# Performance work log

Hardware: AMD Instinct MI355X
Metric: run time of the kernel (lower is better)

Reference implementation:

```python
import jax, jax.numpy as jnp
from jax import lax
import numpy as np

B_, T_ = 16, 8
H_, W_ = 14, 14
h_, w_ = 3, 3
N_ = h_ * w_
CB, C_, D_ = 1024, 512, 128


def setup_inputs():
    key = jax.random.key(0)
    ks = jax.random.split(key, 16)
    rn = lambda i, shp, s=0.02: jax.random.normal(ks[i], shp, dtype=jnp.float32) * s
    z = lambda *s: jnp.zeros(s, jnp.float32)
    o = lambda *s: jnp.ones(s, jnp.float32)
    return {
        'x': jax.random.normal(ks[0], (B_ * T_, CB, H_, W_), dtype=jnp.float32),
        'W_proj': rn(1, (C_, CB)), 'b_proj': z(C_),
        'W_attn': rn(2, (N_, C_)),
        'W_gf': rn(3, (D_, C_)), 'b_gf': z(D_),
        'g1': o(N_, D_), 'beta1': z(N_, D_), 'g2': o(N_, D_), 'beta2': z(N_, D_),
        'W_ih': rn(4, (4 * D_, D_)), 'W_hh': rn(5, (4 * D_, D_)), 'b_ih': z(4 * D_), 'b_hh': z(4 * D_),
        'W_pred': rn(6, (4, D_)), 'b_pred': z(4), 'alpha': jnp.full((4,), 0.5, jnp.float32),
        'W_kp1': rn(7, (C_, H_ * W_)), 'b_kp1': z(C_),
        'Wq': rn(8, (C_, C_)), 'Wk': rn(9, (C_, C_)), 'Wv': rn(10, (C_, C_)), 'Wu': rn(11, (C_, C_)), 'b_u': z(C_),
        'W_gih': rn(12, (3 * C_, C_)), 'W_ghh': rn(13, (3 * C_, C_)), 'b_gih': z(3 * C_), 'b_ghh': z(3 * C_),
        'W_back': rn(14, (CB, C_)), 'b_back': z(CB),
    }


def _ln(x, g, b, eps=1e-5):
    m = x.mean(-1, keepdims=True)
    v = x.var(-1, keepdims=True)
    return (x - m) / jnp.sqrt(v + eps) * g + b


def _forward(x, W_proj, b_proj, W_attn, W_gf, b_gf, g1, beta1, g2, beta2, W_ih, W_hh, b_ih, b_hh, W_pred, b_pred, alpha, W_kp1, b_kp1, Wq, Wk, Wv, Wu, b_u, W_gih, W_ghh, b_gih, b_ghh, W_back, b_back):
    BT = x.shape[0]
    # 1x1 conv projection backbone_dim -> node_dim (project_at_input)  [BT, C, H, W]
    feat = jnp.einsum('oc,bchw->bohw', W_proj, x) + b_proj[None, :, None, None]
    # offset generator: per-node attention pooling over space (GloRe-style)
    logits = jnp.einsum('nc,bchw->bnhw', W_attn, feat).reshape(BT, N_, H_ * W_)
    attw = jax.nn.softmax(logits, axis=-1).reshape(BT, N_, H_, W_)
    gf = jnp.einsum('bnhw,bchw->bnc', attw, feat)  # [BT, N, C]
    gf = _ln(gf @ W_gf.T + b_gf, g1, beta1)  # [BT, N, D]
    # temporal LSTM over T, batched over (B, node)
    xs = gf.reshape(B_, T_, N_, D_).transpose(1, 0, 2, 3).reshape(T_, B_ * N_, D_)
    def lstm_step(carry, xt):
        hp, cp = carry
        gates = xt @ W_ih.T + b_ih + hp @ W_hh.T + b_hh
        i, f, gg, oo = jnp.split(gates, 4, axis=-1)
        c = jax.nn.sigmoid(f) * cp + jax.nn.sigmoid(i) * jnp.tanh(gg)
        hn = jax.nn.sigmoid(oo) * jnp.tanh(c)
        return (hn, c), hn
    h0 = jnp.zeros((B_ * N_, D_), xs.dtype)
    _, ys = lax.scan(lstm_step, (h0, h0), xs)
    ys = ys.reshape(T_, B_, N_, D_).transpose(1, 0, 2, 3).reshape(BT, N_, D_)
    off = (_ln(ys, g2, beta2) @ W_pred.T + b_pred) * alpha  # [BT, N, 4]
    # grid anchors (init_regions='grid'): centers at (k+0.5)*H/h
    ph0 = (jnp.arange(h_, dtype=x.dtype) + 0.5) * (H_ / h_)
    pw0 = (jnp.arange(w_, dtype=x.dtype) + 0.5) * (W_ / w_)
    ch = jnp.repeat(ph0, w_)[None] + off[..., 0]
    cw = jnp.tile(pw0, h_)[None] + off[..., 1]
    sh = (H_ / h_) * jnp.exp(off[..., 2])
    sw = (W_ / w_) * jnp.exp(off[..., 3])
    rel_h = (jnp.arange(h_, dtype=x.dtype) + 0.5) / h_ - 0.5
    rel_w = (jnp.arange(w_, dtype=x.dtype) + 0.5) / w_ - 0.5
    pos_h = ch[..., None] + sh[..., None] * rel_h  # [BT, N, h]
    pos_w = cw[..., None] + sw[..., None] * rel_w  # [BT, N, w]
    grid_h = jnp.arange(H_, dtype=x.dtype)
    grid_w = jnp.arange(W_, dtype=x.dtype)
    kh = jax.nn.relu(1.0 - jnp.abs(pos_h[..., None] - grid_h))  # [BT, N, h, H] linear-interp kernels
    kw = jax.nn.relu(1.0 - jnp.abs(pos_w[..., None] - grid_w))  # [BT, N, w, W]
    # differentiable crop: sample h x w region per node, pool to node vector
    t1 = jnp.einsum('bniH,bcHL->bnicL', kh, feat)
    samp = jnp.einsum('bnicL,bnjL->bnicj', t1, kw).mean(axis=(2, 4))  # [BT, N, C]
    # kernel-location embedding (kernel_projection1), combine_by_sum
    kern2d = jnp.einsum('bniH,bnjL->bnHL', kh, kw).reshape(BT, N_, H_ * W_)
    nodes = samp + kern2d @ W_kp1.T + b_kp1
    # RSTG: spatial message passing on fully-connected node graph
    nd = nodes.reshape(B_, T_, N_, C_)
    q = nd @ Wq.T
    k = nd @ Wk.T
    v = nd @ Wv.T
    att = jax.nn.softmax(jnp.einsum('btic,btjc->btij', q, k) / jnp.sqrt(jnp.asarray(C_, x.dtype)), axis=-1)
    agg = jnp.einsum('btij,btjc->btic', att, v)
    nd = nd + jax.nn.relu(agg @ Wu.T + b_u)
    # RSTG: temporal GRU per node
    def gru_step(hp, xt):
        gi = xt @ W_gih.T + b_gih
        gh = hp @ W_ghh.T + b_ghh
        ir, iz, ig = jnp.split(gi, 3, axis=-1)
        hr, hz, hg = jnp.split(gh, 3, axis=-1)
        r = jax.nn.sigmoid(ir + hr)
        zz = jax.nn.sigmoid(iz + hz)
        n = jnp.tanh(ig + r * hg)
        hn = (1.0 - zz) * n + zz * hp
        return hn, hn
    g0 = jnp.zeros((B_, N_, C_), x.dtype)
    _, hs = lax.scan(gru_step, g0, nd.transpose(1, 0, 2, 3))
    out_nodes = hs.transpose(1, 0, 2, 3).reshape(BT, N_, C_)
    # remap node states back to the spatial map with the same kernels
    khs = kh.sum(2)  # [BT, N, H]
    kws = kw.sum(2)  # [BT, N, W]
    num = jnp.einsum('bnc,bnH,bnL->bcHL', out_nodes, khs, kws)
    den = jnp.einsum('bnH,bnL->bHL', khs, kws) + 1e-6
    out_map = num / den[:, None]
    # project back node_dim -> backbone_dim (project_back_i3d_linear), residual add
    return x + jnp.einsum('oc,bchw->bohw', W_back, out_map) + b_back[None, :, None, None]


def reference(x, W_proj, b_proj, W_attn, W_gf, b_gf, g1, beta1, g2, beta2, W_ih, W_hh, b_ih, b_hh, W_pred, b_pred, alpha, W_kp1, b_kp1, Wq, Wk, Wv, Wu, b_u, W_gih, W_ghh, b_gih, b_ghh, W_back, b_back):
    return _forward(x, W_proj, b_proj, W_attn, W_gf, b_gf, g1, beta1, g2, beta2, W_ih, W_hh, b_ih, b_hh, W_pred, b_pred, alpha, W_kp1, b_kp1, Wq, Wk, Wv, Wu, b_u, W_gih, W_ghh, b_gih, b_ghh, W_back, b_back)
```

## Files before the change

kernel.cpp:

```cpp
#include <hip/hip_runtime.h>

typedef unsigned short u16;
typedef __attribute__((ext_vector_type(8))) u16 b16x8;
typedef __attribute__((ext_vector_type(4))) float f32x4;

static constexpr int HWn = 196;
static constexpr int NN  = 9;
static constexpr int Cn  = 512;
static constexpr int CBn = 1024;
static constexpr int Dn  = 128;
static constexpr int BTn = 128;

__device__ __forceinline__ float sigm(float x) { return 1.f / (1.f + expf(-x)); }

__device__ __forceinline__ u16 f2bf(float f) {
  unsigned int u = __builtin_bit_cast(unsigned int, f);
  u = (u + 0x7fff + ((u >> 16) & 1)) >> 16;
  return (u16)u;
}

__device__ __forceinline__ float waveSum(float v) {
#pragma unroll
  for (int o = 32; o > 0; o >>= 1) v += __shfl_down(v, o, 64);
  return v;
}
__device__ __forceinline__ float waveMax(float v) {
#pragma unroll
  for (int o = 32; o > 0; o >>= 1) v = fmaxf(v, __shfl_down(v, o, 64));
  return v;
}
__device__ __forceinline__ float blockSum(float v, float* red) {
  const int lane = threadIdx.x & 63, wid = threadIdx.x >> 6;
  const int nw = blockDim.x >> 6;
  v = waveSum(v);
  __syncthreads();
  if (lane == 0) red[wid] = v;
  __syncthreads();
  float r = 0.f;
  for (int i = 0; i < nw; ++i) r += red[i];
  return r;
}
__device__ __forceinline__ float blockMax(float v, float* red) {
  const int lane = threadIdx.x & 63, wid = threadIdx.x >> 6;
  const int nw = blockDim.x >> 6;
  v = waveMax(v);
  __syncthreads();
  if (lane == 0) red[wid] = v;
  __syncthreads();
  float r = -3.4e38f;
  for (int i = 0; i < nw; ++i) r = fmaxf(r, red[i]);
  return r;
}

__global__ __launch_bounds__(256) void k_cast(const float* __restrict__ in,
                                              u16* __restrict__ out, int n) {
  const int i = (blockIdx.x * 256 + threadIdx.x) * 4;
  if (i < n) {
    const float4 v = *(const float4*)&in[i];
    out[i + 0] = f2bf(v.x); out[i + 1] = f2bf(v.y);
    out[i + 2] = f2bf(v.z); out[i + 3] = f2bf(v.w);
  }
}

__global__ __launch_bounds__(256) void k_xt(const float* __restrict__ x,
                                            u16* __restrict__ xT) {
  __shared__ u16 T[64][201];
  const int bt = blockIdx.x, c0 = blockIdx.y * 64, tid = threadIdx.x;
  const float* xb = x + ((size_t)bt * CBn + c0) * HWn;
  for (int idx = tid; idx < 64 * HWn; idx += 256)
    T[idx / HWn][idx % HWn] = f2bf(xb[idx]);
  __syncthreads();
  unsigned int* xTu = (unsigned int*)(xT + ((size_t)bt * HWn) * CBn + c0);
  for (int idx = tid; idx < HWn * 32; idx += 256) {
    const int hw = idx >> 5, j = idx & 31;
    const unsigned int lo = T[2 * j][hw], hi = T[2 * j + 1][hw];
    xTu[(size_t)hw * (CBn / 2) + j] = lo | (hi << 16);
  }
}

template <int MODE>
__global__ __launch_bounds__(256) void k_mm128(const u16* __restrict__ A,
                                               const u16* __restrict__ B,
                                               const float* __restrict__ bias,
                                               const float* __restrict__ xres,
                                               float* __restrict__ C,
                                               const int M, const int N, const int K) {
  __shared__ __align__(16) u16 As[128 * 64];
  __shared__ __align__(16) u16 Bs[128 * 64];
  const int tid = threadIdx.x;
  const int lane = tid & 63;
  const int w = tid >> 6, wr = w >> 1, wc = w & 1;
  const int m0 = blockIdx.x * 128, n0 = blockIdx.y * 128;

  int srow[4], slds[4], sc16[4];
#pragma unroll
  for (int i = 0; i < 4; ++i) {
    const int chunk = i * 256 + tid;
    const int row = chunk >> 3, c16 = chunk & 7;
    srow[i] = row; sc16[i] = c16;
    slds[i] = row * 64 + ((c16 ^ (row & 7)) << 3);
  }
  uint4 ar[4], br[4];
#pragma unroll
  for (int i = 0; i < 4; ++i) {
    ar[i] = *(const uint4*)(A + (size_t)(m0 + srow[i]) * K + sc16[i] * 8);
    br[i] = *(const uint4*)(B + (size_t)(n0 + srow[i]) * K + sc16[i] * 8);
  }

  int fa[4][2], fb[4][2];
#pragma unroll
  for (int q = 0; q < 4; ++q)
#pragma unroll
    for (int ks = 0; ks < 2; ++ks) {
      const int rowa = wr * 64 + q * 16 + (lane & 15);
      fa[q][ks] = rowa * 64 + (((ks * 4 + (lane >> 4)) ^ (rowa & 7)) << 3);
      const int rowb = wc * 64 + q * 16 + (lane & 15);
      fb[q][ks] = rowb * 64 + (((ks * 4 + (lane >> 4)) ^ (rowb & 7)) << 3);
    }

  f32x4 acc[4][4];
#pragma unroll
  for (int a = 0; a < 4; ++a)
#pragma unroll
    for (int b = 0; b < 4; ++b) acc[a][b] = f32x4{0.f, 0.f, 0.f, 0.f};

  for (int k0 = 0; k0 < K; k0 += 64) {
    __syncthreads();
#pragma unroll
    for (int i = 0; i < 4; ++i) {
      *(uint4*)&As[slds[i]] = ar[i];
      *(uint4*)&Bs[slds[i]] = br[i];
    }
    __syncthreads();
    const int kn = k0 + 64;
    if (kn < K) {
#pragma unroll
      for (int i = 0; i < 4; ++i) {
        ar[i] = *(const uint4*)(A + (size_t)(m0 + srow[i]) * K + kn + sc16[i] * 8);
        br[i] = *(const uint4*)(B + (size_t)(n0 + srow[i]) * K + kn + sc16[i] * 8);
      }
    }
    b16x8 af[4][2], bg[4][2];
#pragma unroll
    for (int q = 0; q < 4; ++q)
#pragma unroll
      for (int ks = 0; ks < 2; ++ks) {
        af[q][ks] = *(const b16x8*)&As[fa[q][ks]];
        bg[q][ks] = *(const b16x8*)&Bs[fb[q][ks]];
      }
#pragma unroll
    for (int ks = 0; ks < 2; ++ks)
#pragma unroll
      for (int mi = 0; mi < 4; ++mi)
#pragma unroll
        for (int nj = 0; nj < 4; ++nj)
          asm volatile("v_mfma_f32_16x16x32_bf16 %0, %1, %2, %0"
                       : "+v"(acc[mi][nj])
                       : "v"(af[mi][ks]), "v"(bg[nj][ks]));
  }

#pragma unroll
  for (int nj = 0; nj < 4; ++nj) {
    const int n = n0 + wc * 64 + nj * 16 + (lane & 15);
    const float bv = bias[n];
#pragma unroll
    for (int mi = 0; mi < 4; ++mi) {
#pragma unroll
      for (int r = 0; r < 4; ++r) {
        const int m = m0 + wr * 64 + mi * 16 + (lane >> 4) * 4 + r;
        if (MODE == 0) {
          C[(size_t)m * N + n] = acc[mi][nj][r] + bv;
        } else {
          const int b = m / HWn, hw = m - b * HWn;
          const size_t adr = ((size_t)b * CBn + n) * HWn + hw;
          C[adr] = xres[adr] + acc[mi][nj][r] + bv;
        }
      }
    }
  }
}

template <int BIAS, int RELU, int RESID>
__global__ __launch_bounds__(256) void k_gemm(const float* __restrict__ A,
                                              const float* __restrict__ W,
                                              const float* __restrict__ bias,
                                              const float* __restrict__ resid,
                                              float* __restrict__ C,
                                              int M, int N, int K) {
  __shared__ __align__(16) float As[16][68];
  __shared__ __align__(16) float Ws[16][68];
  const int m0 = blockIdx.x * 64, n0 = blockIdx.y * 64;
  const int tid = threadIdx.x, tn = tid & 15, tm = tid >> 4;
  const int lr = tid >> 2, lc4 = (tid & 3) << 2;
  float acc[4][4] = {};
  for (int k0 = 0; k0 < K; k0 += 16) {
    float4 a = make_float4(0.f, 0.f, 0.f, 0.f);
    if (m0 + lr < M) a = *(const float4*)&A[(size_t)(m0 + lr) * K + k0 + lc4];
    As[lc4 + 0][lr] = a.x; As[lc4 + 1][lr] = a.y; As[lc4 + 2][lr] = a.z; As[lc4 + 3][lr] = a.w;
    const float4 w = *(const float4*)&W[(size_t)(n0 + lr) * K + k0 + lc4];
    Ws[lc4 + 0][lr] = w.x; Ws[lc4 + 1][lr] = w.y; Ws[lc4 + 2][lr] = w.z; Ws[lc4 + 3][lr] = w.w;
    __syncthreads();
#pragma unroll
    for (int k = 0; k < 16; ++k) {
      const float4 a4 = *(const float4*)&As[k][tm << 2];
      const float4 b4 = *(const float4*)&Ws[k][tn << 2];
      const float av[4] = {a4.x, a4.y, a4.z, a4.w};
      const float bv[4] = {b4.x, b4.y, b4.z, b4.w};
#pragma unroll
      for (int i = 0; i < 4; ++i)
#pragma unroll
        for (int j = 0; j < 4; ++j) acc[i][j] += av[i] * bv[j];
    }
    __syncthreads();
  }
#pragma unroll
  for (int i = 0; i < 4; ++i) {
    const int m = m0 + tm * 4 + i;
    if (m >= M) continue;
    const int n = n0 + tn * 4;
    float4 v = make_float4(acc[i][0], acc[i][1], acc[i][2], acc[i][3]);
    if (BIAS) { v.x += bias[n]; v.y += bias[n + 1]; v.z += bias[n + 2]; v.w += bias[n + 3]; }
    if (RELU) {
      v.x = fmaxf(v.x, 0.f); v.y = fmaxf(v.y, 0.f);
      v.z = fmaxf(v.z, 0.f); v.w = fmaxf(v.w, 0.f);
    }
    if (RESID) {
      const float4 rr = *(const float4*)&resid[(size_t)m * N + n];
      v.x += rr.x; v.y += rr.y; v.z += rr.z; v.w += rr.w;
    }
    *(float4*)&C[(size_t)m * N + n] = v;
  }
}

__global__ __launch_bounds__(256) void k_attnpool(const float* __restrict__ feat,
                                                  const float* __restrict__ Wattn,
                                                  float* __restrict__ attw) {
  __shared__ float S[HWn][65];
  __shared__ float Wa[NN][64];
  __shared__ float L[NN][HWn];
  __shared__ float red[4];
  const int bt = blockIdx.x, tid = threadIdx.x;
  float lacc[NN];
#pragma unroll
  for (int n = 0; n < NN; ++n) lacc[n] = 0.f;
  const float* fb = feat + (size_t)bt * HWn * Cn;
  const int srow = tid >> 4, sc4 = (tid & 15) << 2;
  for (int c0 = 0; c0 < Cn; c0 += 64) {
    for (int rr = srow; rr < HWn; rr += 16) {
      const float4 f = *(const float4*)&fb[(size_t)rr * Cn + c0 + sc4];
      S[rr][sc4] = f.x; S[rr][sc4 + 1] = f.y; S[rr][sc4 + 2] = f.z; S[rr][sc4 + 3] = f.w;
    }
    for (int idx = tid; idx < NN * 64; idx += 256)
      Wa[idx >> 6][idx & 63] = Wattn[(size_t)(idx >> 6) * Cn + c0 + (idx & 63)];
    __syncthreads();
    if (tid < HWn) {
      for (int c = 0; c < 64; ++c) {
        const float s = S[tid][c];
#pragma unroll
        for (int n = 0; n < NN; ++n) lacc[n] += Wa[n][c] * s;
      }
    }
    __syncthreads();
  }
  if (tid < HWn)
#pragma unroll
    for (int n = 0; n < NN; ++n) L[n][tid] = lacc[n];
  __syncthreads();
  for (int n = 0; n < NN; ++n) {
    const float v = (tid < HWn) ? L[n][tid] : -3.4e38f;
    const float mx = blockMax(v, red);
    const float e = (tid < HWn) ? expf(v - mx) : 0.f;
    const float s = blockSum(e, red);
    if (tid < HWn) attw[((size_t)bt * NN + n) * HWn + tid] = e / s;
  }
}

__global__ __launch_bounds__(256) void k_gf(const float* __restrict__ feat,
                                            const float* __restrict__ attw,
                                            float* __restrict__ gf) {
  __shared__ float aw[NN][HWn];
  const int bt = blockIdx.x, tid = threadIdx.x;
  for (int idx = tid; idx < NN * HWn; idx += 256)
    aw[idx / HWn][idx % HWn] = attw[(size_t)bt * NN * HWn + idx];
  __syncthreads();
  float a0[NN] = {}, a1[NN] = {};
  const float* fb = feat + (size_t)bt * HWn * Cn;
  for (int hw = 0; hw < HWn; ++hw) {
    const float f0 = fb[(size_t)hw * Cn + tid];
    const float f1 = fb[(size_t)hw * Cn + tid + 256];
#pragma unroll
    for (int n = 0; n < NN; ++n) {
      const float w = aw[n][hw];
      a0[n] += w * f0; a1[n] += w * f1;
    }
  }
#pragma unroll
  for (int n = 0; n < NN; ++n) {
    gf[((size_t)bt * NN + n) * Cn + tid] = a0[n];
    gf[((size_t)bt * NN + n) * Cn + tid + 256] = a1[n];
  }
}

__global__ __launch_bounds__(128) void k_gfln(const float* __restrict__ gf,
                                              const float* __restrict__ Wgf,
                                              const float* __restrict__ bgf,
                                              const float* __restrict__ g1,
                                              const float* __restrict__ beta1,
                                              float* __restrict__ gf2) {
  __shared__ __align__(16) float src[Cn];
  __shared__ float red[4];
  const int row = blockIdx.x;
  const int n = row % NN;
  const int tid = threadIdx.x;
  for (int i = tid; i < Cn; i += 128) src[i] = gf[(size_t)row * Cn + i];
  __syncthreads();
  float acc = bgf[tid];
  const float* wr = Wgf + (size_t)tid * Cn;
  for (int c = 0; c < Cn; c += 4) {
    const float4 w = *(const float4*)&wr[c];
    acc += w.x * src[c] + w.y * src[c + 1] + w.z * src[c + 2] + w.w * src[c + 3];
  }
  const float mean = blockSum(acc, red) * (1.f / 128.f);
  const float d = acc - mean;
  const float var = blockSum(d * d, red) * (1.f / 128.f);
  gf2[(size_t)row * Dn + tid] =
      d * rsqrtf(var + 1e-5f) * g1[n * Dn + tid] + beta1[n * Dn + tid];
}

__global__ __launch_bounds__(256) void k_lstm(const float* __restrict__ xW,
                                              const float* __restrict__ Whh,
                                              const float* __restrict__ bhh,
                                              float* __restrict__ ys) {
  __shared__ __align__(16) float h[Dn];
  __shared__ float cc[Dn];
  __shared__ float gates[4 * Dn];
  const int blk = blockIdx.x, b = blk / NN, n = blk % NN;
  const int tid = threadIdx.x;
  if (tid < Dn) { h[tid] = 0.f; cc[tid] = 0.f; }
  __syncthreads();
  for (int t = 0; t < 8; ++t) {
    const int bt = b * 8 + t;
    const size_t xrow = ((size_t)bt * NN + n) * (4 * Dn);
#pragma unroll
    for (int gq = 0; gq < 2; ++gq) {
      const int g = tid + gq * 256;
      float acc = xW[xrow + g] + bhh[g];
      const float* wr = Whh + (size_t)g * Dn;
#pragma unroll 8
      for (int d = 0; d < Dn; d += 4) {
        const float4 w = *(const float4*)&wr[d];
        acc += w.x * h[d] + w.y * h[d + 1] + w.z * h[d + 2] + w.w * h[d + 3];
      }
      gates[g] = acc;
    }
    __syncthreads();
    if (tid < Dn) {
      const float ig = sigm(gates[tid]);
      const float fg = sigm(gates[Dn + tid]);
      const float gg = tanhf(gates[2 * Dn + tid]);
      const float og = sigm(gates[3 * Dn + tid]);
      const float cn = fg * cc[tid] + ig * gg;
      const float hn = og * tanhf(cn);
      cc[tid] = cn; h[tid] = hn;
      ys[((size_t)bt * NN + n) * Dn + tid] = hn;
    }
    __syncthreads();
  }
}

__global__ __launch_bounds__(128) void k_off(const float* __restrict__ ys,
                                             const float* __restrict__ g2,
                                             const float* __restrict__ beta2,
                                             const float* __restrict__ Wpred,
                                             const float* __restrict__ bpred,
                                             const float* __restrict__ alpha,
                                             float* __restrict__ khs,
                                             float* __restrict__ kws) {
  __shared__ float red[4];
  __shared__ float cpar[4];
  const int row = blockIdx.x;
  const int n = row % NN;
  const int tid = threadIdx.x;
  const float y = ys[(size_t)row * Dn + tid];
  const float mean = blockSum(y, red) * (1.f / 128.f);
  const float d = y - mean;
  const float var = blockSum(d * d, red) * (1.f / 128.f);
  const float v = d * rsqrtf(var + 1e-5f) * g2[n * Dn + tid] + beta2[n * Dn + tid];
  const float o0 = blockSum(v * Wpred[0 * Dn + tid], red);
  const float o1 = blockSum(v * Wpred[1 * Dn + tid], red);
  const float o2 = blockSum(v * Wpred[2 * Dn + tid], red);
  const float o3 = blockSum(v * Wpred[3 * Dn + tid], red);
  if (tid == 0) {
    const float f0 = (o0 + bpred[0]) * alpha[0];
    const float f1 = (o1 + bpred[1]) * alpha[1];
    const float f2 = (o2 + bpred[2]) * alpha[2];
    const float f3 = (o3 + bpred[3]) * alpha[3];
    const float ph0 = ((n / 3) + 0.5f) * (14.f / 3.f);
    const float pw0 = ((n % 3) + 0.5f) * (14.f / 3.f);
    cpar[0] = ph0 + f0;
    cpar[1] = pw0 + f1;
    cpar[2] = (14.f / 3.f) * expf(f2);
    cpar[3] = (14.f / 3.f) * expf(f3);
  }
  __syncthreads();
  if (tid < 14) {
    float s = 0.f;
#pragma unroll
    for (int i = 0; i < 3; ++i) {
      const float rel = (i + 0.5f) / 3.f - 0.5f;
      const float p = cpar[0] + cpar[2] * rel;
      s += fmaxf(1.f - fabsf(p - (float)tid), 0.f);
    }
    khs[(size_t)row * 14 + tid] = s;
  } else if (tid < 28) {
    const int H = tid - 14;
    float s = 0.f;
#pragma unroll
    for (int i = 0; i < 3; ++i) {
      const float rel = (i + 0.5f) / 3.f - 0.5f;
      const float p = cpar[1] + cpar[3] * rel;
      s += fmaxf(1.f - fabsf(p - (float)H), 0.f);
    }
    kws[(size_t)row * 14 + H] = s;
  }
}

__global__ __launch_bounds__(256) void k_wkp1t(const float* __restrict__ Wkp1,
                                               float* __restrict__ wkT) {
  const int hw = blockIdx.x, c = threadIdx.x;
  wkT[(size_t)hw * Cn + c] = Wkp1[(size_t)c * HWn + hw];
  wkT[(size_t)hw * Cn + c + 256] = Wkp1[(size_t)(c + 256) * HWn + hw];
}

__global__ __launch_bounds__(256) void k_nodes(const float* __restrict__ feat,
                                               const float* __restrict__ wkT,
                                               const float* __restrict__ khs,
                                               const float* __restrict__ kws,
                                               const float* __restrict__ bkp1,
                                               float* __restrict__ nodes) {
  __shared__ float kh[NN][14], kw[NN][14];
  const int bt = blockIdx.x, tid = threadIdx.x;
  if (tid < NN * 14) {
    kh[tid / 14][tid % 14] = khs[(size_t)bt * NN * 14 + tid];
    kw[tid / 14][tid % 14] = kws[(size_t)bt * NN * 14 + tid];
  }
  __syncthreads();
  float a0[NN] = {}, a1[NN] = {};
  const float* fb = feat + (size_t)bt * HWn * Cn;
  for (int hw = 0; hw < HWn; ++hw) {
    const int Hh = hw / 14, Ll = hw % 14;
    const float f0 = fb[(size_t)hw * Cn + tid] * (1.f / 9.f) + wkT[(size_t)hw * Cn + tid];
    const float f1 = fb[(size_t)hw * Cn + tid + 256] * (1.f / 9.f) + wkT[(size_t)hw * Cn + tid + 256];
#pragma unroll
    for (int n = 0; n < NN; ++n) {
      const float w = kh[n][Hh] * kw[n][Ll];
      a0[n] += w * f0; a1[n] += w * f1;
    }
  }
#pragma unroll
  for (int n = 0; n < NN; ++n) {
    nodes[((size_t)bt * NN + n) * Cn + tid] = a0[n] + bkp1[tid];
    nodes[((size_t)bt * NN + n) * Cn + tid + 256] = a1[n] + bkp1[tid + 256];
  }
}

__global__ __launch_bounds__(256) void k_att(const float* __restrict__ q,
                                             const float* __restrict__ k,
                                             const float* __restrict__ v,
                                             float* __restrict__ agg) {
  __shared__ __align__(16) float qs[NN][Cn];
  __shared__ __align__(16) float ks[NN][Cn];
  __shared__ __align__(16) float vs[NN][Cn];
  __shared__ float s[NN][NN];
  const int bt = blockIdx.x, tid = threadIdx.x;
  const size_t base = (size_t)bt * NN * Cn;
  for (int idx = tid; idx < NN * Cn; idx += 256) {
    qs[idx / Cn][idx % Cn] = q[base + idx];
    ks[idx / Cn][idx % Cn] = k[base + idx];
    vs[idx / Cn][idx % Cn] = v[base + idx];
  }
  __syncthreads();
  if (tid < NN * NN) {
    const int i = tid / NN, j = tid % NN;
    float acc = 0.f;
    for (int c = 0; c < Cn; c += 4) {
      const float4 qa = *(const float4*)&qs[i][c];
      const float4 kb = *(const float4*)&ks[j][c];
      acc += qa.x * kb.x + qa.y * kb.y + qa.z * kb.z + qa.w * kb.w;
    }
    s[i][j] = acc * 0.044194173824159216f;
  }
  __syncthreads();
  if (tid < NN) {
    float mx = -3.4e38f;
#pragma unroll
    for (int j = 0; j < NN; ++j) mx = fmaxf(mx, s[tid][j]);
    float sum = 0.f;
#pragma unroll
    for (int j = 0; j < NN; ++j) { const float e = expf(s[tid][j] - mx); s[tid][j] = e; sum += e; }
    const float inv = 1.f / sum;
#pragma unroll
    for (int j = 0; j < NN; ++j) s[tid][j] *= inv;
  }
  __syncthreads();
  for (int c = tid; c < Cn; c += 256) {
#pragma unroll
    for (int i = 0; i < NN; ++i) {
      float acc = 0.f;
#pragma unroll
      for (int j = 0; j < NN; ++j) acc += s[i][j] * vs[j][c];
      agg[((size_t)bt * NN + i) * Cn + c] = acc;
    }
  }
}

template <int T0>
__global__ __launch_bounds__(256) void k_gruupd(const float* __restrict__ gi,
                                                const float* __restrict__ gh,
                                                const float* __restrict__ bghh,
                                                float* __restrict__ hgru,
                                                float* __restrict__ out_nodes,
                                                int t) {
  const int idx = blockIdx.x * 256 + threadIdx.x;
  const int row = idx >> 9, d = idx & 511;
  const int b = row / NN, n = row % NN;
  const size_t girow = ((size_t)(b * 8 + t) * NN + n) * (3 * Cn);
  const float ir = gi[girow + d], iz = gi[girow + Cn + d], ig = gi[girow + 2 * Cn + d];
  float hr, hz, hg, hp;
  if (T0) {
    hr = bghh[d]; hz = bghh[Cn + d]; hg = bghh[2 * Cn + d]; hp = 0.f;
  } else {
    const size_t gr = (size_t)row * (3 * Cn);
    hr = gh[gr + d]; hz = gh[gr + Cn + d]; hg = gh[gr + 2 * Cn + d];
    hp = hgru[(size_t)row * Cn + d];
  }
  const float rg = sigm(ir + hr);
  const float zg = sigm(iz + hz);
  const float ng = tanhf(ig + rg * hg);
  const float h = (1.f - zg) * ng + zg * hp;
  hgru[(size_t)row * Cn + d] = h;
  out_nodes[((size_t)(b * 8 + t) * NN + n) * Cn + d] = h;
}

__global__ __launch_bounds__(256) void k_remap(const float* __restrict__ out_nodes,
                                               const float* __restrict__ khs,
                                               const float* __restrict__ kws,
                                               u16* __restrict__ om) {
  __shared__ __align__(16) float on[NN][Cn];
  __shared__ float kh[NN][14], kw[NN][14];
  const int bt = blockIdx.x, tid = threadIdx.x;
  for (int idx = tid; idx < NN * Cn; idx += 256)
    on[idx / Cn][idx % Cn] = out_nodes[(size_t)bt * NN * Cn + idx];
  if (tid < NN * 14) {
    kh[tid / 14][tid % 14] = khs[(size_t)bt * NN * 14 + tid];
    kw[tid / 14][tid % 14] = kws[(size_t)bt * NN * 14 + tid];
  }
  __syncthreads();
  for (int hw = 0; hw < HWn; ++hw) {
    const int Hh = hw / 14, Ll = hw % 14;
    float w[NN];
    float den = 1e-6f;
#pragma unroll
    for (int n = 0; n < NN; ++n) { w[n] = kh[n][Hh] * kw[n][Ll]; den += w[n]; }
    const float inv = 1.f / den;
    float s0 = 0.f, s1 = 0.f;
#pragma unroll
    for (int n = 0; n < NN; ++n) {
      s0 += on[n][tid] * w[n];
      s1 += on[n][tid + 256] * w[n];
    }
    om[((size_t)bt * HWn + hw) * Cn + tid] = f2bf(s0 * inv);
    om[((size_t)bt * HWn + hw) * Cn + tid + 256] = f2bf(s1 * inv);
  }
}

extern "C" void kernel_launch(void* const* d_in, const int* in_sizes, int n_in,
                              void* d_out, int out_size, void* d_ws, size_t ws_size,
                              hipStream_t stream) {
  const float* x      = (const float*)d_in[0];
  const float* W_proj = (const float*)d_in[1];
  const float* b_proj = (const float*)d_in[2];
  const float* W_attn = (const float*)d_in[3];
  const float* W_gf   = (const float*)d_in[4];
  const float* b_gf   = (const float*)d_in[5];
  const float* g1     = (const float*)d_in[6];
  const float* beta1  = (const float*)d_in[7];
  const float* g2     = (const float*)d_in[8];
  const float* beta2  = (const float*)d_in[9];
  const float* W_ih   = (const float*)d_in[10];
  const float* W_hh   = (const float*)d_in[11];
  const float* b_ih   = (const float*)d_in[12];
  const float* b_hh   = (const float*)d_in[13];
  const float* W_pred = (const float*)d_in[14];
  const float* b_pred = (const float*)d_in[15];
  const float* alpha  = (const float*)d_in[16];
  const float* W_kp1  = (const float*)d_in[17];
  const float* b_kp1  = (const float*)d_in[18];
  const float* Wq     = (const float*)d_in[19];
  const float* Wk     = (const float*)d_in[20];
  const float* Wv     = (const float*)d_in[21];
  const float* Wu     = (const float*)d_in[22];
  const float* b_u    = (const float*)d_in[23];
  const float* W_gih  = (const float*)d_in[24];
  const float* W_ghh  = (const float*)d_in[25];
  const float* b_gih  = (const float*)d_in[26];
  const float* b_ghh  = (const float*)d_in[27];
  const float* W_back = (const float*)d_in[28];
  const float* b_back = (const float*)d_in[29];
  float* out = (float*)d_out;

  float* ws = (float*)d_ws;
  float* feat = ws;
  u16* om16 = (u16*)feat;
  float* pool = ws + 12845056;
  u16* xT = (u16*)pool;
  size_t off = 0;
  float* attw      = pool + off; off += (size_t)BTn * NN * HWn;
  float* gf        = pool + off; off += (size_t)BTn * NN * Cn;
  float* gf2       = pool + off; off += (size_t)BTn * NN * Dn;
  float* xW        = pool + off; off += (size_t)BTn * NN * 512;
  float* ys        = pool + off; off += (size_t)BTn * NN * Dn;
  float* khs       = pool + off; off += (size_t)BTn * NN * 14;
  float* kws       = pool + off; off += (size_t)BTn * NN * 14;
  float* nodes     = pool + off; off += (size_t)BTn * NN * Cn;
  float* qb        = pool + off; off += (size_t)BTn * NN * Cn;
  float* kb        = pool + off; off += (size_t)BTn * NN * Cn;
  float* vb        = pool + off; off += (size_t)BTn * NN * Cn;
  float* aggb      = pool + off; off += (size_t)BTn * NN * Cn;
  float* nd2       = pool + off; off += (size_t)BTn * NN * Cn;
  float* gi        = pool + off; off += (size_t)BTn * NN * 3 * Cn;
  float* hgru      = pool + off; off += (size_t)144 * Cn;
  float* gh        = pool + off; off += (size_t)144 * 3 * Cn;
  float* wkT       = pool + off; off += (size_t)HWn * Cn;
  float* out_nodes = pool + off; off += (size_t)BTn * NN * Cn;
  u16* Wpb = (u16*)(ws + 25690112);
  u16* Wbb = (u16*)(ws + 25952256);

  k_cast<<<512, 256, 0, stream>>>(W_proj, Wpb, 524288);
  k_cast<<<512, 256, 0, stream>>>(W_back, Wbb, 524288);
  k_xt<<<dim3(128, 16), 256, 0, stream>>>(x, xT);
  k_mm128<0><<<dim3(196, 4), 256, 0, stream>>>(xT, Wpb, b_proj, nullptr, feat, 25088, 512, 1024);
  k_attnpool<<<BTn, 256, 0, stream>>>(feat, W_attn, attw);
  k_gf<<<BTn, 256, 0, stream>>>(feat, attw, gf);
  k_gfln<<<BTn * NN, 128, 0, stream>>>(gf, W_gf, b_gf, g1, beta1, gf2);
  k_gemm<1, 0, 0><<<dim3(18, 8), 256, 0, stream>>>(gf2, W_ih, b_ih, nullptr, xW, 1152, 512, 128);
  k_lstm<<<144, 256, 0, stream>>>(xW, W_hh, b_hh, ys);
  k_off<<<BTn * NN, 128, 0, stream>>>(ys, g2, beta2, W_pred, b_pred, alpha, khs, kws);
  k_wkp1t<<<HWn, 256, 0, stream>>>(W_kp1, wkT);
  k_nodes<<<BTn, 256, 0, stream>>>(feat, wkT, khs, kws, b_kp1, nodes);
  k_gemm<0, 0, 0><<<dim3(18, 8), 256, 0, stream>>>(nodes, Wq, nullptr, nullptr, qb, 1152, 512, 512);
  k_gemm<0, 0, 0><<<dim3(18, 8), 256, 0, stream>>>(nodes, Wk, nullptr, nullptr, kb, 1152, 512, 512);
  k_gemm<0, 0, 0><<<dim3(18, 8), 256, 0, stream>>>(nodes, Wv, nullptr, nullptr, vb, 1152, 512, 512);
  k_att<<<BTn, 256, 0, stream>>>(qb, kb, vb, aggb);
  k_gemm<1, 1, 1><<<dim3(18, 8), 256, 0, stream>>>(aggb, Wu, b_u, nodes, nd2, 1152, 512, 512);
  k_gemm<1, 0, 0><<<dim3(18, 24), 256, 0, stream>>>(nd2, W_gih, b_gih, nullptr, gi, 1152, 1536, 512);
  for (int t = 0; t < 8; ++t) {
    if (t > 0)
      k_gemm<1, 0, 0><<<dim3(3, 24), 256, 0, stream>>>(hgru, W_ghh, b_ghh, nullptr, gh, 144, 1536, 512);
    if (t == 0)
      k_gruupd<1><<<288, 256, 0, stream>>>(gi, gh, b_ghh, hgru, out_nodes, t);
    else
      k_gruupd<0><<<288, 256, 0, stream>>>(gi, gh, b_ghh, hgru, out_nodes, t);
  }
  k_remap<<<BTn, 256, 0, stream>>>(out_nodes, khs, kws, om16);
  k_mm128<1><<<dim3(196, 8), 256, 0, stream>>>(om16, Wbb, b_back, x, out, 25088, 1024, 512);
}
```

Measured before the change: 1.377 ms.

## Route mid-size fp32 GEMMs through bf16 MFMA kernel with fused epilogues

Replaces the scalar fp32 tiled GEMM used for the LSTM input projection, Q/K/V/U projections, GRU input gates and per-step GRU hidden GEMM with the bf16 MFMA 128x128 kernel. Adds one combined cast kernel for the mid-stage weights, makes producer kernels also emit bf16 copies of their outputs, and adds an M-bound clamp plus a bias/ReLU/residual epilogue that writes bf16. The MODE 1 back-projection epilogue swaps the MFMA operand order so each lane writes consecutive spatial positions. The gain is tensor-core throughput and less traffic; the cost is extra cast work, bf16 precision loss in the recurrent GRU, and underfilled grids (36 to 108 blocks).

Result: slower. 1.431 ms (+3.9%).

```diff
diff --git a/kernel.cpp b/kernel.cpp
--- a/kernel.cpp
+++ b/kernel.cpp
@@ -62,6 +62,30 @@
   }
 }
 
+__global__ __launch_bounds__(256) void k_castall(const float* __restrict__ wq,
+                                                 const float* __restrict__ wk,
+                                                 const float* __restrict__ wv,
+                                                 const float* __restrict__ wu,
+                                                 const float* __restrict__ wgih,
+                                                 const float* __restrict__ wghh,
+                                                 const float* __restrict__ wih,
+                                                 u16* __restrict__ dst) {
+  const int i = (blockIdx.x * 256 + threadIdx.x) * 4;
+  if (i >= 2686976) return;
+  const float* src;
+  int o = i;
+  if (i < 262144) { src = wq; }
+  else if (i < 524288)  { src = wk;   o = i - 262144; }
+  else if (i < 786432)  { src = wv;   o = i - 524288; }
+  else if (i < 1048576) { src = wu;   o = i - 786432; }
+  else if (i < 1835008) { src = wgih; o = i - 1048576; }
+  else if (i < 2621440) { src = wghh; o = i - 1835008; }
+  else                  { src = wih;  o = i - 2621440; }
+  const float4 v = *(const float4*)&src[o];
+  dst[i + 0] = f2bf(v.x); dst[i + 1] = f2bf(v.y);
+  dst[i + 2] = f2bf(v.z); dst[i + 3] = f2bf(v.w);
+}
+
 __global__ __launch_bounds__(256) void k_xt(const float* __restrict__ x,
                                             u16* __restrict__ xT) {
   __shared__ u16 T[64][201];
@@ -82,7 +106,7 @@
 __global__ __launch_bounds__(256) void k_mm128(const u16* __restrict__ A,
                                                const u16* __restrict__ B,
                                                const float* __restrict__ bias,
-                                               const float* __restrict__ xres,
+                                               const float* __restrict__ resid,
                                                float* __restrict__ C,
                                                const int M, const int N, const int K) {
   __shared__ __align__(16) u16 As[128 * 64];
@@ -92,19 +116,21 @@
   const int w = tid >> 6, wr = w >> 1, wc = w & 1;
   const int m0 = blockIdx.x * 128, n0 = blockIdx.y * 128;
 
-  int srow[4], slds[4], sc16[4];
+  int srowA[4], srowB[4], slds[4], sc16[4];
 #pragma unroll
   for (int i = 0; i < 4; ++i) {
     const int chunk = i * 256 + tid;
     const int row = chunk >> 3, c16 = chunk & 7;
-    srow[i] = row; sc16[i] = c16;
+    srowA[i] = min(m0 + row, M - 1);
+    srowB[i] = n0 + row;
+    sc16[i] = c16;
     slds[i] = row * 64 + ((c16 ^ (row & 7)) << 3);
   }
   uint4 ar[4], br[4];
 #pragma unroll
   for (int i = 0; i < 4; ++i) {
-    ar[i] = *(const uint4*)(A + (size_t)(m0 + srow[i]) * K + sc16[i] * 8);
-    br[i] = *(const uint4*)(B + (size_t)(n0 + srow[i]) * K + sc16[i] * 8);
+    ar[i] = *(const uint4*)(A + (size_t)srowA[i] * K + sc16[i] * 8);
+    br[i] = *(const uint4*)(B + (size_t)srowB[i] * K + sc16[i] * 8);
   }
 
   int fa[4][2], fb[4][2];
@@ -136,8 +162,8 @@
     if (kn < K) {
 #pragma unroll
       for (int i = 0; i < 4; ++i) {
-        ar[i] = *(const uint4*)(A + (size_t)(m0 + srow[i]) * K + kn + sc16[i] * 8);
-        br[i] = *(const uint4*)(B + (size_t)(n0 + srow[i]) * K + kn + sc16[i] * 8);
+        ar[i] = *(const uint4*)(A + (size_t)srowA[i] * K + kn + sc16[i] * 8);
+        br[i] = *(const uint4*)(B + (size_t)srowB[i] * K + kn + sc16[i] * 8);
       }
     }
     b16x8 af[4][2], bg[4][2];
@@ -153,82 +179,54 @@
 #pragma unroll
       for (int mi = 0; mi < 4; ++mi)
 #pragma unroll
-        for (int nj = 0; nj < 4; ++nj)
-          asm volatile("v_mfma_f32_16x16x32_bf16 %0, %1, %2, %0"
-                       : "+v"(acc[mi][nj])
-                       : "v"(af[mi][ks]), "v"(bg[nj][ks]));
-  }
-
-#pragma unroll
-  for (int nj = 0; nj < 4; ++nj) {
-    const int n = n0 + wc * 64 + nj * 16 + (lane & 15);
-    const float bv = bias[n];
-#pragma unroll
-    for (int mi = 0; mi < 4; ++mi) {
+        for (int nj = 0; nj < 4; ++nj) {
+          if (MODE == 1)
+            asm volatile("v_mfma_f32_16x16x32_bf16 %0, %1, %2, %0"
+                         : "+v"(acc[mi][nj])
+                         : "v"(bg[nj][ks]), "v"(af[mi][ks]));
+          else
+            asm volatile("v_mfma_f32_16x16x32_bf16 %0, %1, %2, %0"
+                         : "+v"(acc[mi][nj])
+                         : "v"(af[mi][ks]), "v"(bg[nj][ks]));
+        }
+  }
+
+  if (MODE == 1) {
+#pragma unroll
+    for (int nj = 0; nj < 4; ++nj) {
 #pragma unroll
       for (int r = 0; r < 4; ++r) {
-        const int m = m0 + wr * 64 + mi * 16 + (lane >> 4) * 4 + r;
-        if (MODE == 0) {
-          C[(size_t)m * N + n] = acc[mi][nj][r] + bv;
-        } else {
+        const int n = n0 + wc * 64 + nj * 16 + (lane >> 4) * 4 + r;
+        const float bv = bias[n];
+#pragma unroll
+        for (int mi = 0; mi < 4; ++mi) {
+          const int m = m0 + wr * 64 + mi * 16 + (lane & 15);
           const int b = m / HWn, hw = m - b * HWn;
           const size_t adr = ((size_t)b * CBn + n) * HWn + hw;
-          C[adr] = xres[adr] + acc[mi][nj][r] + bv;
+          C[adr] = resid[adr] + acc[mi][nj][r] + bv;
         }
       }
     }
-  }
-}
-
-template <int BIAS, int RELU, int RESID>
-__global__ __launch_bounds__(256) void k_gemm(const float* __restrict__ A,
-                                              const float* __restrict__ W,
-                                              const float* __restrict__ bias,
-                                              const float* __restrict__ resid,
-                                              float* __restrict__ C,
-                                              int M, int N, int K) {
-  __shared__ __align__(16) float As[16][68];
-  __shared__ __align__(16) float Ws[16][68];
-  const int m0 = blockIdx.x * 64, n0 = blockIdx.y * 64;
-  const int tid = threadIdx.x, tn = tid & 15, tm = tid >> 4;
-  const int lr = tid >> 2, lc4 = (tid & 3) << 2;
-  float acc[4][4] = {};
-  for (int k0 = 0; k0 < K; k0 += 16) {
-    float4 a = make_float4(0.f, 0.f, 0.f, 0.f);
-    if (m0 + lr < M) a = *(const float4*)&A[(size_t)(m0 + lr) * K + k0 + lc4];
-    As[lc4 + 0][lr] = a.x; As[lc4 + 1][lr] = a.y; As[lc4 + 2][lr] = a.z; As[lc4 + 3][lr] = a.w;
-    const float4 w = *(const float4*)&W[(size_t)(n0 + lr) * K + k0 + lc4];
-    Ws[lc4 + 0][lr] = w.x; Ws[lc4 + 1][lr] = w.y; Ws[lc4 + 2][lr] = w.z; Ws[lc4 + 3][lr] = w.w;
-    __syncthreads();
-#pragma unroll
-    for (int k = 0; k < 16; ++k) {
-      const float4 a4 = *(const float4*)&As[k][tm << 2];
-      const float4 b4 = *(const float4*)&Ws[k][tn << 2];
-      const float av[4] = {a4.x, a4.y, a4.z, a4.w};
-      const float bv[4] = {b4.x, b4.y, b4.z, b4.w};
-#pragma unroll
-      for (int i = 0; i < 4; ++i)
-#pragma unroll
-        for (int j = 0; j < 4; ++j) acc[i][j] += av[i] * bv[j];
-    }
-    __syncthreads();
-  }
-#pragma unroll
-  for (int i = 0; i < 4; ++i) {
-    const int m = m0 + tm * 4 + i;
-    if (m >= M) continue;
-    const int n = n0 + tn * 4;
-    float4 v = make_float4(acc[i][0], acc[i][1], acc[i][2], acc[i][3]);
-    if (BIAS) { v.x += bias[n]; v.y += bias[n + 1]; v.z += bias[n + 2]; v.w += bias[n + 3]; }
-    if (RELU) {
-      v.x = fmaxf(v.x, 0.f); v.y = fmaxf(v.y, 0.f);
-      v.z = fmaxf(v.z, 0.f); v.w = fmaxf(v.w, 0.f);
-    }
-    if (RESID) {
-      const float4 rr = *(const float4*)&resid[(size_t)m * N + n];
-      v.x += rr.x; v.y += rr.y; v.z += rr.z; v.w += rr.w;
-    }
-    *(float4*)&C[(size_t)m * N + n] = v;
+  } else {
+#pragma unroll
+    for (int nj = 0; nj < 4; ++nj) {
+      const int n = n0 + wc * 64 + nj * 16 + (lane & 15);
+      const float bv = (MODE == 3) ? bias[n] : (bias ? bias[n] : 0.f);
+#pragma unroll
+      for (int mi = 0; mi < 4; ++mi) {
+#pragma unroll
+        for (int r = 0; r < 4; ++r) {
+          const int m = m0 + wr * 64 + mi * 16 + (lane >> 4) * 4 + r;
+          if (m >= M) continue;
+          if (MODE == 0) {
+            C[(size_t)m * N + n] = acc[mi][nj][r] + bv;
+          } else {
+            const float val = resid[(size_t)m * N + n] + fmaxf(acc[mi][nj][r] + bv, 0.f);
+            ((u16*)C)[(size_t)m * N + n] = f2bf(val);
+          }
+        }
+      }
+    }
   }
 }
 
@@ -306,7 +304,7 @@
                                               const float* __restrict__ bgf,
                                               const float* __restrict__ g1,
                                               const float* __restrict__ beta1,
-                                              float* __restrict__ gf2) {
+                                              u16* __restrict__ gf2b) {
   __shared__ __align__(16) float src[Cn];
   __shared__ float red[4];
   const int row = blockIdx.x;
@@ -323,8 +321,8 @@
   const float mean = blockSum(acc, red) * (1.f / 128.f);
   const float d = acc - mean;
   const float var = blockSum(d * d, red) * (1.f / 128.f);
-  gf2[(size_t)row * Dn + tid] =
-      d * rsqrtf(var + 1e-5f) * g1[n * Dn + tid] + beta1[n * Dn + tid];
+  gf2b[(size_t)row * Dn + tid] =
+      f2bf(d * rsqrtf(var + 1e-5f) * g1[n * Dn + tid] + beta1[n * Dn + tid]);
 }
 
 __global__ __launch_bounds__(256) void k_lstm(const float* __restrict__ xW,
@@ -437,7 +435,8 @@
                                                const float* __restrict__ khs,
                                                const float* __restrict__ kws,
                                                const float* __restrict__ bkp1,
-                                               float* __restrict__ nodes) {
+                                               float* __restrict__ nodes,
+                                               u16* __restrict__ nodesb) {
   __shared__ float kh[NN][14], kw[NN][14];
   const int bt = blockIdx.x, tid = threadIdx.x;
   if (tid < NN * 14) {
@@ -459,15 +458,19 @@
   }
 #pragma unroll
   for (int n = 0; n < NN; ++n) {
-    nodes[((size_t)bt * NN + n) * Cn + tid] = a0[n] + bkp1[tid];
-    nodes[((size_t)bt * NN + n) * Cn + tid + 256] = a1[n] + bkp1[tid + 256];
+    const float v0 = a0[n] + bkp1[tid];
+    const float v1 = a1[n] + bkp1[tid + 256];
+    nodes[((size_t)bt * NN + n) * Cn + tid] = v0;
+    nodes[((size_t)bt * NN + n) * Cn + tid + 256] = v1;
+    nodesb[((size_t)bt * NN + n) * Cn + tid] = f2bf(v0);
+    nodesb[((size_t)bt * NN + n) * Cn + tid + 256] = f2bf(v1);
   }
 }
 
 __global__ __launch_bounds__(256) void k_att(const float* __restrict__ q,
                                              const float* __restrict__ k,
                                              const float* __restrict__ v,
-                                             float* __restrict__ agg) {
+                                             u16* __restrict__ aggb) {
   __shared__ __align__(16) float qs[NN][Cn];
   __shared__ __align__(16) float ks[NN][Cn];
   __shared__ __align__(16) float vs[NN][Cn];
@@ -509,7 +512,7 @@
       float acc = 0.f;
 #pragma unroll
       for (int j = 0; j < NN; ++j) acc += s[i][j] * vs[j][c];
-      agg[((size_t)bt * NN + i) * Cn + c] = acc;
+      aggb[((size_t)bt * NN + i) * Cn + c] = f2bf(acc);
     }
   }
 }
@@ -519,6 +522,7 @@
                                                 const float* __restrict__ gh,
                                                 const float* __restrict__ bghh,
                                                 float* __restrict__ hgru,
+                                                u16* __restrict__ hb,
                                                 float* __restrict__ out_nodes,
                                                 int t) {
   const int idx = blockIdx.x * 256 + threadIdx.x;
@@ -539,6 +543,7 @@
   const float ng = tanhf(ig + rg * hg);
   const float h = (1.f - zg) * ng + zg * hp;
   hgru[(size_t)row * Cn + d] = h;
+  hb[(size_t)row * Cn + d] = f2bf(h);
   out_nodes[((size_t)(b * 8 + t) * NN + n) * Cn + d] = h;
 }
 
@@ -617,7 +622,7 @@
   size_t off = 0;
   float* attw      = pool + off; off += (size_t)BTn * NN * HWn;
   float* gf        = pool + off; off += (size_t)BTn * NN * Cn;
-  float* gf2       = pool + off; off += (size_t)BTn * NN * Dn;
+  u16*   gf2b      = (u16*)(pool + off); off += (size_t)BTn * NN * Dn;
   float* xW        = pool + off; off += (size_t)BTn * NN * 512;
   float* ys        = pool + off; off += (size_t)BTn * NN * Dn;
   float* khs       = pool + off; off += (size_t)BTn * NN * 14;
@@ -626,41 +631,52 @@
   float* qb        = pool + off; off += (size_t)BTn * NN * Cn;
   float* kb        = pool + off; off += (size_t)BTn * NN * Cn;
   float* vb        = pool + off; off += (size_t)BTn * NN * Cn;
-  float* aggb      = pool + off; off += (size_t)BTn * NN * Cn;
-  float* nd2       = pool + off; off += (size_t)BTn * NN * Cn;
   float* gi        = pool + off; off += (size_t)BTn * NN * 3 * Cn;
   float* hgru      = pool + off; off += (size_t)144 * Cn;
   float* gh        = pool + off; off += (size_t)144 * 3 * Cn;
   float* wkT       = pool + off; off += (size_t)HWn * Cn;
   float* out_nodes = pool + off; off += (size_t)BTn * NN * Cn;
+  u16* midw    = (u16*)(pool + off); off += 1343488;
+  u16* nodesb  = (u16*)(pool + off); off += 294912;
+  u16* nd2b    = (u16*)(pool + off); off += 294912;
+  u16* aggb16  = (u16*)(pool + off); off += 294912;
+  u16* hb      = (u16*)(pool + off); off += 36864;
+  u16* Wqb   = midw;
+  u16* Wkb   = midw + 262144;
+  u16* Wvb   = midw + 524288;
+  u16* Wub   = midw + 786432;
+  u16* Wgihb = midw + 1048576;
+  u16* Wghhb = midw + 1835008;
+  u16* Wihb  = midw + 2621440;
   u16* Wpb = (u16*)(ws + 25690112);
-  u16* Wbb = (u16*)(ws + 25952256);
+  u16* Wbb = (u16*)(ws + 25690112 + 262144);
 
   k_cast<<<512, 256, 0, stream>>>(W_proj, Wpb, 524288);
   k_cast<<<512, 256, 0, stream>>>(W_back, Wbb, 524288);
   k_xt<<<dim3(128, 16), 256, 0, stream>>>(x, xT);
   k_mm128<0><<<dim3(196, 4), 256, 0, stream>>>(xT, Wpb, b_proj, nullptr, feat, 25088, 512, 1024);
+  k_castall<<<2624, 256, 0, stream>>>(Wq, Wk, Wv, Wu, W_gih, W_ghh, W_ih, midw);
   k_attnpool<<<BTn, 256, 0, stream>>>(feat, W_attn, attw);
   k_gf<<<BTn, 256, 0, stream>>>(feat, attw, gf);
-  k_gfln<<<BTn * NN, 128, 0, stream>>>(gf, W_gf, b_gf, g1, beta1, gf2);
-  k_gemm<1, 0, 0><<<dim3(18, 8), 256, 0, stream>>>(gf2, W_ih, b_ih, nullptr, xW, 1152, 512, 128);
+  k_gfln<<<BTn * NN, 128, 0, stream>>>(gf, W_gf, b_gf, g1, beta1, gf2b);
+  k_mm128<0><<<dim3(9, 4), 256, 0, stream>>>(gf2b, Wihb, b_ih, nullptr, xW, 1152, 512, 128);
   k_lstm<<<144, 256, 0, stream>>>(xW, W_hh, b_hh, ys);
   k_off<<<BTn * NN, 128, 0, stream>>>(ys, g2, beta2, W_pred, b_pred, alpha, khs, kws);
   k_wkp1t<<<HWn, 256, 0, stream>>>(W_kp1, wkT);
-  k_nodes<<<BTn, 256, 0, stream>>>(feat, wkT, khs, kws, b_kp1, nodes);
-  k_gemm<0, 0, 0><<<dim3(18, 8), 256, 0, stream>>>(nodes, Wq, nullptr, nullptr, qb, 1152, 512, 512);
-  k_gemm<0, 0, 0><<<dim3(18, 8), 256, 0, stream>>>(nodes, Wk, nullptr, nullptr, kb, 1152, 512, 512);
-  k_gemm<0, 0, 0><<<dim3(18, 8), 256, 0, stream>>>(nodes, Wv, nullptr, nullptr, vb, 1152, 512, 512);
-  k_att<<<BTn, 256, 0, stream>>>(qb, kb, vb, aggb);
-  k_gemm<1, 1, 1><<<dim3(18, 8), 256, 0, stream>>>(aggb, Wu, b_u, nodes, nd2, 1152, 512, 512);
-  k_gemm<1, 0, 0><<<dim3(18, 24), 256, 0, stream>>>(nd2, W_gih, b_gih, nullptr, gi, 1152, 1536, 512);
+  k_nodes<<<BTn, 256, 0, stream>>>(feat, wkT, khs, kws, b_kp1, nodes, nodesb);
+  k_mm128<0><<<dim3(9, 4), 256, 0, stream>>>(nodesb, Wqb, nullptr, nullptr, qb, 1152, 512, 512);
+  k_mm128<0><<<dim3(9, 4), 256, 0, stream>>>(nodesb, Wkb, nullptr, nullptr, kb, 1152, 512, 512);
+  k_mm128<0><<<dim3(9, 4), 256, 0, stream>>>(nodesb, Wvb, nullptr, nullptr, vb, 1152, 512, 512);
+  k_att<<<BTn, 256, 0, stream>>>(qb, kb, vb, aggb16);
+  k_mm128<3><<<dim3(9, 4), 256, 0, stream>>>(aggb16, Wub, b_u, nodes, (float*)nd2b, 1152, 512, 512);
+  k_mm128<0><<<dim3(9, 12), 256, 0, stream>>>(nd2b, Wgihb, b_gih, nullptr, gi, 1152, 1536, 512);
   for (int t = 0; t < 8; ++t) {
     if (t > 0)
-      k_gemm<1, 0, 0><<<dim3(3, 24), 256, 0, stream>>>(hgru, W_ghh, b_ghh, nullptr, gh, 144, 1536, 512);
+      k_mm128<0><<<dim3(2, 12), 256, 0, stream>>>(hb, Wghhb, b_ghh, nullptr, gh, 144, 1536, 512);
     if (t == 0)
-      k_gruupd<1><<<288, 256, 0, stream>>>(gi, gh, b_ghh, hgru, out_nodes, t);
+      k_gruupd<1><<<288, 256, 0, stream>>>(gi, gh, b_ghh, hgru, hb, out_nodes, t);
     else
-      k_gruupd<0><<<288, 256, 0, stream>>>(gi, gh, b_ghh, hgru, out_nodes, t);
+      k_gruupd<0><<<288, 256, 0, stream>>>(gi, gh, b_ghh, hgru, hb, out_nodes, t);
   }
   k_remap<<<BTn, 256, 0, stream>>>(out_nodes, khs, kws, om16);
   k_mm128<1><<<dim3(196, 8), 256, 0, stream>>>(om16, Wbb, b_back, x, out, 25088, 1024, 512);
```
